# Optimization experiments

Hardware: AMD Instinct MI355X
Metric: run time of the kernel (lower is better)

The kernel has to match this reference:

```python
import jax, jax.numpy as jnp
from jax import lax
import numpy as np

B, S, MEL = 64, 1024, 60
H, L = 180, 4
FS = 3          # mel_smooth_filter_size (num shifted conv branches)
BLOCKS = 3      # mel_smooth_layers
G = MEL // FS   # 20 output units per grouped conv
POST, OUT = 8192, 300


def setup_inputs() -> dict:
    key = jax.random.key(0)
    ks = jax.random.split(key, 13)
    rn = lambda k, shape, s: jax.random.normal(k, shape, jnp.float32) * s
    x = jax.random.normal(ks[0], (B, S, MEL), jnp.float32)
    lens = jax.random.randint(ks[1], (B,), 1, S + 1)
    conv_w = rn(ks[2], (BLOCKS, FS, G, FS, 5), 0.2)   # per block, per shift: (O=20, I/g=3, k=5)
    conv_b = rn(ks[3], (BLOCKS, FS, G), 0.1)
    lstm_wih0 = rn(ks[4], (4 * H, MEL), 0.08)
    lstm_wih_rest = rn(ks[5], (L - 1, 4 * H, H), 0.08)
    lstm_whh = rn(ks[6], (L, 4 * H, H), 0.08)
    lstm_bih = rn(ks[7], (L, 4 * H), 0.05)
    lstm_bhh = rn(ks[8], (L, 4 * H), 0.05)
    post_w = rn(ks[9], (POST, H), 0.05)
    post_b = rn(ks[10], (POST,), 0.05)
    up_w = rn(ks[11], (OUT, POST), 0.02)
    up_b = rn(ks[12], (OUT,), 0.02)
    return dict(x=x, lens=lens, conv_w=conv_w, conv_b=conv_b,
                lstm_wih0=lstm_wih0, lstm_wih_rest=lstm_wih_rest, lstm_whh=lstm_whh,
                lstm_bih=lstm_bih, lstm_bhh=lstm_bhh,
                post_w=post_w, post_b=post_b, up_w=up_w, up_b=up_b)


def _mel_block(xc, w, b):
    # xc: (B, MEL, S); w: (FS, G, FS, 5); b: (FS, G)
    zrow = jnp.zeros_like(xc[:, :1])
    xs = []
    for i in range(FS - 2):  # shift channels down by i+1
        n = i + 1
        xs.append(jnp.concatenate([jnp.zeros_like(xc[:, :n]), xc[:, :-n]], axis=1))
    xs.append(xc)
    xs.append(jnp.concatenate([xc[:, 1:], zrow], axis=1))  # shift channels up by 1
    outs = []
    for j in range(FS):
        o = lax.conv_general_dilated(xs[j], w[j], (1,), [(2, 2)],
                                     dimension_numbers=('NCH', 'OIH', 'NCH'),
                                     feature_group_count=G)
        outs.append(o + b[j][None, :, None])  # (B, G, S)
    # interleave: out channel FS*i + j = outs[j][:, i]
    return jnp.stack(outs, axis=2).reshape(xc.shape[0], MEL, xc.shape[2])


def _lstm_layer(h_in, wih, whh, bih, bhh):
    # h_in: (B, T, I). Torch gate order: i, f, g, o.
    pre = jnp.einsum('bti,gi->btg', h_in, wih) + (bih + bhh)  # (B, T, 4H)
    pre = pre.transpose(1, 0, 2)  # (T, B, 4H)
    h0 = jnp.zeros((h_in.shape[0], H), h_in.dtype)

    def step(carry, p):
        hh, cc = carry
        gates = p + hh @ whh.T
        i, f, g, o = jnp.split(gates, 4, axis=-1)
        cc = jax.nn.sigmoid(f) * cc + jax.nn.sigmoid(i) * jnp.tanh(g)
        hh = jax.nn.sigmoid(o) * jnp.tanh(cc)
        return (hh, cc), hh

    _, outs = lax.scan(step, (h0, h0), pre)
    return outs.transpose(1, 0, 2)  # (B, T, H)


def reference(x, lens, conv_w, conv_b, lstm_wih0, lstm_wih_rest, lstm_whh,
              lstm_bih, lstm_bhh, post_w, post_b, up_w, up_b):
    xc = x.transpose(0, 2, 1)  # (B, MEL, S)
    for blk in range(BLOCKS):
        shortcut = xc
        xc = _mel_block(xc, conv_w[blk], conv_b[blk]) + shortcut  # resid activation = Identity
    h = xc.transpose(0, 2, 1)  # (B, S, MEL)
    for l in range(L):
        wih = lstm_wih0 if l == 0 else lstm_wih_rest[l - 1]
        h = _lstm_layer(h, wih, lstm_whh[l], lstm_bih[l], lstm_bhh[l])
    idx = jnp.clip(lens - 1, 0, S - 1)
    last = h[jnp.arange(h.shape[0]), idx]  # (B, H)
    post = jax.nn.leaky_relu(last @ post_w.T + post_b, 0.01)  # LeakyReLU default slope
    return post @ up_w.T + up_b  # (B, OUT)
```

## Files before the change

### kernel.cpp

```cpp
#include <hip/hip_runtime.h>
#include <hip/hip_fp16.h>

#define BB 64
#define SS 1024
#define MEL 60
#define HH 180
#define G4 720
#define G4P 768
#define NCG 48
#define NKS 6
#define KP 192
#define NL 4
#define NPOST 8192
#define NOUT 300
#define NOUTP 320
#define KSPL 16
#define TT 128
#define CH 64
#define NCH (SS / CH)
#define KPAIR 96

typedef _Float16 f16x8 __attribute__((ext_vector_type(8)));
typedef float f32x4 __attribute__((ext_vector_type(4)));

#if defined(__has_builtin)
#if __has_builtin(__builtin_amdgcn_fdot2)
#define HAVE_FDOT2 1
#endif
#if __has_builtin(__builtin_amdgcn_rcpf)
#define HAVE_RCPF 1
#endif
#endif
#ifndef HAVE_FDOT2
#define HAVE_FDOT2 0
#endif
#ifndef HAVE_RCPF
#define HAVE_RCPF 0
#endif

__device__ __forceinline__ float fdot2u(unsigned int w, unsigned int h, float acc) {
#if HAVE_FDOT2
    typedef _Float16 h2_t __attribute__((ext_vector_type(2)));
    union U { unsigned int u; h2_t v; };
    U a, b;
    a.u = w; b.u = h;
    return __builtin_amdgcn_fdot2(a.v, b.v, acc, false);
#else
    __half2 aw = *reinterpret_cast<const __half2*>(&w);
    __half2 ah = *reinterpret_cast<const __half2*>(&h);
    acc += __half2float(__low2half(aw)) * __half2float(__low2half(ah));
    acc += __half2float(__high2half(aw)) * __half2float(__high2half(ah));
    return acc;
#endif
}

__device__ __forceinline__ float fast_rcp(float x) {
#if HAVE_RCPF
    return __builtin_amdgcn_rcpf(x);
#else
    return 1.f / x;
#endif
}
__device__ __forceinline__ float fsigm(float x) { return fast_rcp(1.f + __expf(-x)); }
__device__ __forceinline__ float ftanh(float x) { return 1.f - 2.f * fast_rcp(__expf(2.f * x) + 1.f); }

union WU { uint4 u; f16x8 f; };

__global__ void prep_wmf(const float* __restrict__ whh, uint4* __restrict__ wmf) {
    int idx = blockIdx.x * blockDim.x + threadIdx.x;
    int total = NL * NCG * NKS * 64;
    if (idx >= total) return;
    int l = idx / (NCG * NKS * 64);
    int r = idx % (NCG * NKS * 64);
    int cg = r / (NKS * 64);
    int r2 = r % (NKS * 64);
    int ks = r2 / 64, lane = r2 % 64;
    int col = cg * 16 + (lane & 15);
    unsigned short v[8];
    #pragma unroll
    for (int j = 0; j < 8; ++j) {
        int k = ks * 32 + ((lane >> 4) << 3) + j;
        float f = (k < HH && col < G4) ? whh[((size_t)l * G4 + col) * HH + k] : 0.f;
        v[j] = __half_as_ushort(__float2half(f));
    }
    uint4 u;
    u.x = (unsigned)v[0] | ((unsigned)v[1] << 16);
    u.y = (unsigned)v[2] | ((unsigned)v[3] << 16);
    u.z = (unsigned)v[4] | ((unsigned)v[5] << 16);
    u.w = (unsigned)v[6] | ((unsigned)v[7] << 16);
    wmf[idx] = u;
}

__global__ void prep_wih16(const float* __restrict__ wih0, const float* __restrict__ wih_rest,
                           unsigned int* __restrict__ w) {
    int idx = blockIdx.x * blockDim.x + threadIdx.x;
    int total = NL * G4 * KPAIR;
    if (idx >= total) return;
    int l = idx / (G4 * KPAIR);
    int r = idx % (G4 * KPAIR);
    int g = r / KPAIR, kp = r % KPAIR;
    int K = (l == 0) ? MEL : HH;
    const float* src = (l == 0) ? (wih0 + (size_t)g * MEL)
                                : (wih_rest + ((size_t)(l - 1) * G4 + g) * HH);
    float a = 0.f, b = 0.f;
    if (2 * kp < K) { a = src[2 * kp]; b = src[2 * kp + 1]; }
    __half2 h2 = __floats2half2_rn(a, b);
    w[idx] = *(unsigned int*)&h2;
}

__global__ void prep_bsum(const float* __restrict__ bih, const float* __restrict__ bhh,
                          float* __restrict__ bsum) {
    int idx = blockIdx.x * blockDim.x + threadIdx.x;
    if (idx >= NL * G4) return;
    bsum[idx] = bih[idx] + bhh[idx];
}

template <typename TIN>
__global__ __launch_bounds__(256) void mel_block(const TIN* __restrict__ in,
                                                 __half* __restrict__ out,
                                                 const float* __restrict__ w,
                                                 const float* __restrict__ bias) {
    __shared__ float xt[TT + 4][MEL];
    __shared__ float ws[900];
    __shared__ float bs[MEL];
    int bb = blockIdx.x;
    int t0 = blockIdx.y * TT;
    int tid = threadIdx.x;
    const TIN* inb = in + (size_t)bb * SS * MEL;
    for (int idx = tid; idx < (TT + 4) * MEL; idx += 256) {
        int tt = idx / MEL, ch = idx % MEL;
        int t = t0 + tt - 2;
        xt[tt][ch] = (t >= 0 && t < SS) ? (float)inb[(size_t)t * MEL + ch] : 0.f;
    }
    for (int idx = tid; idx < 900; idx += 256) ws[idx] = w[idx];
    if (tid < MEL) bs[tid] = bias[(tid % 3) * 20 + tid / 3];
    __syncthreads();
    for (int idx = tid; idx < TT * MEL; idx += 256) {
        int tt = idx / MEL, ch = idx % MEL;
        int i = ch / 3, j = ch % 3;
        int qb = 3 * i + (j - 1);
        float acc = bs[ch];
        #pragma unroll
        for (int c = 0; c < 3; ++c) {
            int q = qb + c;
            if (q >= 0 && q < MEL) {
                const float* wp = ws + ((j * 20 + i) * 3 + c) * 5;
                #pragma unroll
                for (int k = 0; k < 5; ++k) acc += xt[tt + k][q] * wp[k];
            }
        }
        out[(size_t)bb * SS * MEL + (size_t)(t0 + tt) * MEL + ch] =
            __float2half(acc + xt[tt + 2][ch]);
    }
}

struct GemmArgs {
    const __half* A[16];
    const unsigned int* W[16];
    const float* bs[16];
    __half* C[16];
    size_t cbs[16];
    int K[16];
    int KT[16];
    int t0[16];
};

__global__ __launch_bounds__(256) void gemm_pre(GemmArgs ga) {
    int j = blockIdx.z;
    int K = ga.K[j], KT = ga.KT[j];
    const __half* Ab = ga.A[j] + ((size_t)blockIdx.x * SS + ga.t0[j]) * K;
    __half* Cb = ga.C[j] + (size_t)blockIdx.x * ga.cbs[j];
    const unsigned int* Wj = ga.W[j];
    const float* bsum = ga.bs[j];
    __shared__ unsigned int A16[8][72];
    __shared__ unsigned int W16[8][72];
    int n0 = blockIdx.y * 64;
    int tid = threadIdx.x;
    int tx = tid & 15, ty = tid >> 4;
    int kpl = tid & 7, mg = tid >> 3;
    float acc[4][4];
    #pragma unroll
    for (int i = 0; i < 4; ++i)
        #pragma unroll
        for (int jn = 0; jn < 4; ++jn) acc[i][jn] = 0.f;

    for (int kt = 0; kt < KT; ++kt) {
        int kp = kt * 8 + kpl;
        #pragma unroll
        for (int r = 0; r < 2; ++r) {
            int m = mg + 32 * r;
            unsigned int av = 0u;
            if (2 * kp < K) av = *(const unsigned int*)(Ab + (size_t)m * K + 2 * kp);
            A16[kpl][m] = av;
            int g = n0 + m;
            W16[kpl][m] = (g < G4) ? Wj[(size_t)g * KPAIR + kp] : 0u;
        }
        __syncthreads();
        #pragma unroll
        for (int k = 0; k < 8; ++k) {
            unsigned int a[4], b[4];
            #pragma unroll
            for (int i = 0; i < 4; ++i) a[i] = A16[k][ty + (i << 4)];
            #pragma unroll
            for (int jn = 0; jn < 4; ++jn) b[jn] = W16[k][(tx << 2) + jn];
            #pragma unroll
            for (int i = 0; i < 4; ++i)
                #pragma unroll
                for (int jn = 0; jn < 4; ++jn) acc[i][jn] = fdot2u(b[jn], a[i], acc[i][jn]);
        }
        __syncthreads();
    }
    int g0 = n0 + (tx << 2);
    if (g0 < G4) {
        #pragma unroll
        for (int i = 0; i < 4; ++i) {
            int m = ty + (i << 4);
            __half2 p0 = __floats2half2_rn(acc[i][0] + bsum[g0], acc[i][1] + bsum[g0 + 1]);
            __half2 p1 = __floats2half2_rn(acc[i][2] + bsum[g0 + 2], acc[i][3] + bsum[g0 + 3]);
            *(__half2*)(Cb + (size_t)m * G4 + g0) = p0;
            *(__half2*)(Cb + (size_t)m * G4 + g0 + 2) = p1;
        }
    }
}

struct ScanArgs {
    const __half* pre[NL];
    size_t pbs[NL];
    const uint4* wmf[NL];
    __half* hout[NL];
    float* hst[NL];
    float* cst[NL];
    int t0[NL];
};

__global__ __launch_bounds__(768) __attribute__((amdgpu_waves_per_eu(3, 3)))
void lstm_scan(ScanArgs sa) {
    int j = blockIdx.x / BB, b = blockIdx.x % BB;
    int tid = threadIdx.x;
    int wv = tid >> 6, lane = tid & 63;
    int t0 = sa.t0[j];
    const __half* preb = sa.pre[j] + (size_t)b * sa.pbs[j];
    const uint4* wmf = sa.wmf[j];
    __half* houtb = sa.hout[j] + ((size_t)b * SS + (size_t)t0) * HH;
    float* hstb = sa.hst[j] + b * HH;
    float* cstb = sa.cst[j] + b * HH;

    __shared__ __align__(16) unsigned short hs[KP];
    __shared__ float gates[G4P];

    uint4 wfr[24];
    #pragma unroll
    for (int q = 0; q < 4; ++q)
        #pragma unroll
        for (int ks = 0; ks < NKS; ++ks)
            wfr[q * NKS + ks] = wmf[(((size_t)(wv * 4 + q)) * NKS + ks) * 64 + lane];
    #pragma unroll
    for (int r = 0; r < 24; ++r)
        asm volatile("" : "+v"(wfr[r].x), "+v"(wfr[r].y), "+v"(wfr[r].z), "+v"(wfr[r].w));

    float c = 0.f, hlast = 0.f;
    if (tid < KP) {
        float hv = 0.f;
        if (t0 > 0 && tid < HH) { hv = hstb[tid]; c = cstb[tid]; }
        hs[tid] = __half_as_ushort(__float2half(hv));
    }
    __syncthreads();

    float pc0 = 0.f, pc1 = 0.f, pc2 = 0.f, pc3 = 0.f;
    if (tid < HH) {
        pc0 = __half2float(preb[tid]);
        pc1 = __half2float(preb[HH + tid]);
        pc2 = __half2float(preb[2 * HH + tid]);
        pc3 = __half2float(preb[3 * HH + tid]);
    }

    int hoff = (lane >> 4) << 4;
    for (int t = 0; t < CH; ++t) {
        float pn0 = 0.f, pn1 = 0.f, pn2 = 0.f, pn3 = 0.f;
        if (tid < HH && t + 1 < CH) {
            const __half* pp = preb + (size_t)(t + 1) * G4 + tid;
            pn0 = __half2float(pp[0]);
            pn1 = __half2float(pp[HH]);
            pn2 = __half2float(pp[2 * HH]);
            pn3 = __half2float(pp[3 * HH]);
        }
        f16x8 hf[NKS];
        #pragma unroll
        for (int ks = 0; ks < NKS; ++ks) {
            WU hu;
            hu.u = *(const uint4*)((const char*)hs + ks * 64 + hoff);
            hf[ks] = hu.f;
        }
        f32x4 acc0 = {0.f, 0.f, 0.f, 0.f}, acc1 = acc0, acc2 = acc0, acc3 = acc0;
        #pragma unroll
        for (int ks = 0; ks < NKS; ++ks) {
            WU w0, w1, w2, w3;
            w0.u = wfr[0 * NKS + ks]; w1.u = wfr[1 * NKS + ks];
            w2.u = wfr[2 * NKS + ks]; w3.u = wfr[3 * NKS + ks];
            acc0 = __builtin_amdgcn_mfma_f32_16x16x32_f16(hf[ks], w0.f, acc0, 0, 0, 0);
            acc1 = __builtin_amdgcn_mfma_f32_16x16x32_f16(hf[ks], w1.f, acc1, 0, 0, 0);
            acc2 = __builtin_amdgcn_mfma_f32_16x16x32_f16(hf[ks], w2.f, acc2, 0, 0, 0);
            acc3 = __builtin_amdgcn_mfma_f32_16x16x32_f16(hf[ks], w3.f, acc3, 0, 0, 0);
        }
        if (lane < 16) {
            gates[(wv * 4 + 0) * 16 + lane] = acc0[0];
            gates[(wv * 4 + 1) * 16 + lane] = acc1[0];
            gates[(wv * 4 + 2) * 16 + lane] = acc2[0];
            gates[(wv * 4 + 3) * 16 + lane] = acc3[0];
        }
        __syncthreads();
        if (tid < HH) {
            float gi = gates[tid] + pc0;
            float gf = gates[HH + tid] + pc1;
            float gg = gates[2 * HH + tid] + pc2;
            float go = gates[3 * HH + tid] + pc3;
            float si = fsigm(gi);
            float sf = fsigm(gf);
            float so = fsigm(go);
            float tg = ftanh(gg);
            c = sf * c + si * tg;
            float hn = so * ftanh(c);
            __half hh = __float2half(hn);
            hs[tid] = __half_as_ushort(hh);
            hlast = __half2float(hh);
            houtb[(size_t)t * HH + tid] = hh;
        }
        __syncthreads();
        pc0 = pn0; pc1 = pn1; pc2 = pn2; pc3 = pn3;
    }
    if (tid < HH) { hstb[tid] = hlast; cstb[tid] = c; }
}

__global__ void gather_last(const __half* __restrict__ hfin, const int* __restrict__ lens,
                            float* __restrict__ last) {
    int idx = blockIdx.x * blockDim.x + threadIdx.x;
    if (idx >= BB * HH) return;
    int b = idx / HH, d = idx % HH;
    int t = lens[b] - 1;
    t = t < 0 ? 0 : (t > SS - 1 ? SS - 1 : t);
    last[idx] = __half2float(hfin[((size_t)b * SS + t) * HH + d]);
}

__global__ __launch_bounds__(256) void post_gemm(const float* __restrict__ A,
                                                 const float* __restrict__ Bw,
                                                 const float* __restrict__ pb,
                                                 float* __restrict__ Cb) {
    __shared__ float As[16][68];
    __shared__ float Bs[16][68];
    int n0 = blockIdx.x * 64;
    int tid = threadIdx.x;
    int kk = tid & 15, q = tid >> 4;
    int tx = tid & 15, ty = tid >> 4;
    float acc[4][4];
    #pragma unroll
    for (int i = 0; i < 4; ++i)
        #pragma unroll
        for (int jj = 0; jj < 4; ++jj) acc[i][jj] = 0.f;
    for (int kt = 0; kt < 12; ++kt) {
        int kidx = kt * 16 + kk;
        bool kval = kidx < HH;
        #pragma unroll
        for (int r = 0; r < 4; ++r)
            As[kk][q + (r << 4)] = kval ? A[(size_t)(q + (r << 4)) * HH + kidx] : 0.f;
        #pragma unroll
        for (int r = 0; r < 4; ++r)
            Bs[kk][q + (r << 4)] = kval ? Bw[(size_t)(n0 + q + (r << 4)) * HH + kidx] : 0.f;
        __syncthreads();
        #pragma unroll
        for (int k = 0; k < 16; ++k) {
            float a[4], bv[4];
            #pragma unroll
            for (int i = 0; i < 4; ++i) a[i] = As[k][ty + (i << 4)];
            #pragma unroll
            for (int jj = 0; jj < 4; ++jj) bv[jj] = Bs[k][(tx << 2) + jj];
            #pragma unroll
            for (int i = 0; i < 4; ++i)
                #pragma unroll
                for (int jj = 0; jj < 4; ++jj) acc[i][jj] = fmaf(a[i], bv[jj], acc[i][jj]);
        }
        __syncthreads();
    }
    #pragma unroll
    for (int i = 0; i < 4; ++i) {
        int m = ty + (i << 4);
        #pragma unroll
        for (int jj = 0; jj < 4; ++jj) {
            int g = n0 + (tx << 2) + jj;
            float v = acc[i][jj] + pb[g];
            Cb[(size_t)m * NPOST + g] = v > 0.f ? v : 0.01f * v;
        }
    }
}

__global__ __launch_bounds__(256) void up_gemm(const float* __restrict__ A,
                                               const float* __restrict__ Bw,
                                               float* __restrict__ part) {
    __shared__ float As[16][68];
    __shared__ float Bs[16][68];
    int n0 = blockIdx.x * 64;
    int k0 = blockIdx.y * (NPOST / KSPL);
    float* Pb = part + (size_t)blockIdx.y * BB * NOUTP;
    int tid = threadIdx.x;
    int kk = tid & 15, q = tid >> 4;
    int tx = tid & 15, ty = tid >> 4;
    float acc[4][4];
    #pragma unroll
    for (int i = 0; i < 4; ++i)
        #pragma unroll
        for (int jj = 0; jj < 4; ++jj) acc[i][jj] = 0.f;
    for (int kt = 0; kt < (NPOST / KSPL) / 16; ++kt) {
        int kidx = k0 + kt * 16 + kk;
        #pragma unroll
        for (int r = 0; r < 4; ++r)
            As[kk][q + (r << 4)] = A[(size_t)(q + (r << 4)) * NPOST + kidx];
        #pragma unroll
        for (int r = 0; r < 4; ++r) {
            int g = n0 + q + (r << 4);
            Bs[kk][q + (r << 4)] = (g < NOUT) ? Bw[(size_t)g * NPOST + kidx] : 0.f;
        }
        __syncthreads();
        #pragma unroll
        for (int k = 0; k < 16; ++k) {
            float a[4], bv[4];
            #pragma unroll
            for (int i = 0; i < 4; ++i) a[i] = As[k][ty + (i << 4)];
            #pragma unroll
            for (int jj = 0; jj < 4; ++jj) bv[jj] = Bs[k][(tx << 2) + jj];
            #pragma unroll
            for (int i = 0; i < 4; ++i)
                #pragma unroll
                for (int jj = 0; jj < 4; ++jj) acc[i][jj] = fmaf(a[i], bv[jj], acc[i][jj]);
        }
        __syncthreads();
    }
    #pragma unroll
    for (int i = 0; i < 4; ++i) {
        int m = ty + (i << 4);
        #pragma unroll
        for (int jj = 0; jj < 4; ++jj) {
            int g = n0 + (tx << 2) + jj;
            Pb[(size_t)m * NOUTP + g] = acc[i][jj];
        }
    }
}

__global__ void up_reduce(const float* __restrict__ part, const float* __restrict__ ub,
                          float* __restrict__ out) {
    int idx = blockIdx.x * blockDim.x + threadIdx.x;
    if (idx >= BB * NOUT) return;
    int b = idx / NOUT, o = idx % NOUT;
    float acc = ub[o];
    #pragma unroll
    for (int ks = 0; ks < KSPL; ++ks)
        acc += part[((size_t)ks * BB + b) * NOUTP + o];
    out[(size_t)b * NOUT + o] = acc;
}

extern "C" void kernel_launch(void* const* d_in, const int* in_sizes, int n_in,
                              void* d_out, int out_size, void* d_ws, size_t ws_size,
                              hipStream_t stream) {
    const float* x        = (const float*)d_in[0];
    const int*   lens     = (const int*)d_in[1];
    const float* conv_w   = (const float*)d_in[2];
    const float* conv_b   = (const float*)d_in[3];
    const float* wih0     = (const float*)d_in[4];
    const float* wih_rest = (const float*)d_in[5];
    const float* whh      = (const float*)d_in[6];
    const float* bih      = (const float*)d_in[7];
    const float* bhh      = (const float*)d_in[8];
    const float* post_w   = (const float*)d_in[9];
    const float* post_b   = (const float*)d_in[10];
    const float* up_w     = (const float*)d_in[11];
    const float* up_b     = (const float*)d_in[12];
    float* out = (float*)d_out;
    (void)in_sizes; (void)n_in; (void)out_size;

    auto pad = [](size_t v) { return (v + 255) & ~(size_t)255; };
    const size_t szMel   = (size_t)BB * SS * MEL * 2;
    const size_t szH     = (size_t)BB * SS * HH * 2;
    const size_t szPre0  = (size_t)BB * SS * G4 * 2;
    const size_t szSlot  = (size_t)BB * CH * G4 * 2;
    const size_t szWmf   = (size_t)NL * NCG * NKS * 64 * 16;
    const size_t szWih   = (size_t)NL * G4 * KPAIR * 4;
    const size_t szBsum  = (size_t)NL * G4 * 4;
    const size_t szState = (size_t)NL * BB * HH * 4;
    const size_t szLast  = (size_t)BB * HH * 4;
    const size_t szPost  = (size_t)BB * NPOST * 4;
    const size_t szPart  = (size_t)KSPL * BB * NOUTP * 4;

    size_t commonSmall = pad(szWmf) + pad(szWih) + pad(szBsum) + 2 * pad(szState) +
                         pad(szLast) + pad(szPost) + pad(szPart) + 4096;
    size_t need1 = pad(szMel) + 4 * pad(szH) + pad(szPre0) + 3 * pad(szSlot) + commonSmall;
    size_t need2 = pad(szMel) + 4 * pad(szH) + 4 * pad(szSlot) + commonSmall;
    int tier = (ws_size >= need1) ? 1 : ((ws_size >= need2) ? 2 : 3);

    char* wsp = (char*)d_ws;
    size_t off = 0;
    auto alloc = [&](size_t bytes) -> void* {
        void* p = wsp + off;
        off = (off + bytes + 255) & ~(size_t)255;
        return p;
    };

    __half* melF = (__half*)alloc(szMel);
    __half* hbuf[NL];
    if (tier <= 2) {
        for (int l = 0; l < NL; ++l) hbuf[l] = (__half*)alloc(szH);
    } else {
        __half* p0 = (__half*)alloc(szH);
        __half* p1 = (__half*)alloc(szH);
        hbuf[0] = p0; hbuf[1] = p1; hbuf[2] = p0; hbuf[3] = p1;
    }
    __half* pre0 = nullptr;
    __half* slot[NL] = {nullptr, nullptr, nullptr, nullptr};
    if (tier == 1) {
        pre0 = (__half*)alloc(szPre0);
        for (int l = 1; l < NL; ++l) slot[l] = (__half*)alloc(szSlot);
    } else if (tier == 2) {
        for (int l = 0; l < NL; ++l) slot[l] = (__half*)alloc(szSlot);
    } else {
        slot[0] = (__half*)alloc(szSlot);
        for (int l = 1; l < NL; ++l) slot[l] = slot[0];
    }
    uint4* wmf = (uint4*)alloc(szWmf);
    unsigned int* wih16 = (unsigned int*)alloc(szWih);
    float* bsum  = (float*)alloc(szBsum);
    float* hstates = (float*)alloc(szState);
    float* cstates = (float*)alloc(szState);
    float* lastb = (float*)alloc(szLast);
    float* postb = (float*)alloc(szPost);
    float* partb = (float*)alloc(szPart);

    prep_wmf<<<(NL * NCG * NKS * 64 + 255) / 256, 256, 0, stream>>>(whh, wmf);
    prep_wih16<<<(NL * G4 * KPAIR + 255) / 256, 256, 0, stream>>>(wih0, wih_rest, wih16);
    prep_bsum<<<(NL * G4 + 255) / 256, 256, 0, stream>>>(bih, bhh, bsum);

    {
        __half* m0 = hbuf[0];
        __half* m1 = (__half*)((char*)hbuf[0] + pad(szMel));
        mel_block<float><<<dim3(BB, SS / TT), 256, 0, stream>>>(x, m0, conv_w + 0 * 900, conv_b + 0 * 60);
        mel_block<__half><<<dim3(BB, SS / TT), 256, 0, stream>>>(m0, m1, conv_w + 1 * 900, conv_b + 1 * 60);
        mel_block<__half><<<dim3(BB, SS / TT), 256, 0, stream>>>(m1, melF, conv_w + 2 * 900, conv_b + 2 * 60);
    }

    auto setGemmJob = [&](GemmArgs& ga, int nj, int l, int c) {
        ga.A[nj]  = (l == 0) ? melF : hbuf[l - 1];
        ga.K[nj]  = (l == 0) ? MEL : HH;
        ga.KT[nj] = (l == 0) ? 4 : 12;
        ga.W[nj]  = wih16 + (size_t)l * G4 * KPAIR;
        ga.bs[nj] = bsum + l * G4;
        if (tier == 1 && l == 0) {
            ga.C[nj] = pre0 + (size_t)c * CH * G4;
            ga.cbs[nj] = (size_t)SS * G4;
        } else {
            ga.C[nj] = slot[l];
            ga.cbs[nj] = (size_t)CH * G4;
        }
        ga.t0[nj] = c * CH;
    };
    auto setScanJob = [&](ScanArgs& sa, int nj, int l, int c) {
        if (tier == 1 && l == 0) {
            sa.pre[nj] = pre0 + (size_t)c * CH * G4;
            sa.pbs[nj] = (size_t)SS * G4;
        } else {
            sa.pre[nj] = slot[l];
            sa.pbs[nj] = (size_t)CH * G4;
        }
        sa.wmf[nj]  = wmf + (size_t)l * NCG * NKS * 64;
        sa.hout[nj] = hbuf[l];
        sa.hst[nj]  = hstates + (size_t)l * BB * HH;
        sa.cst[nj]  = cstates + (size_t)l * BB * HH;
        sa.t0[nj]   = c * CH;
    };

    if (tier <= 2) {
        if (tier == 1) {
            GemmArgs ga{};
            for (int c = 0; c < NCH; ++c) setGemmJob(ga, c, 0, c);
            gemm_pre<<<dim3(BB, 12, NCH), 256, 0, stream>>>(ga);
        }
        int lmin = (tier == 1) ? 1 : 0;
        for (int w = 0; w < NCH + NL - 1; ++w) {
            GemmArgs ga{};
            int njg = 0;
            for (int l = lmin; l < NL; ++l) {
                int c = w - l;
                if (c < 0 || c >= NCH) continue;
                setGemmJob(ga, njg++, l, c);
            }
            if (njg) gemm_pre<<<dim3(BB, 12, njg), 256, 0, stream>>>(ga);
            ScanArgs sa{};
            int njs = 0;
            for (int l = 0; l < NL; ++l) {
                int c = w - l;
                if (c < 0 || c >= NCH) continue;
                setScanJob(sa, njs++, l, c);
            }
            if (njs) lstm_scan<<<dim3(njs * BB), 768, 0, stream>>>(sa);
        }
    } else {
        for (int l = 0; l < NL; ++l) {
            for (int c = 0; c < NCH; ++c) {
                GemmArgs ga{}; ScanArgs sa{};
                setGemmJob(ga, 0, l, c);
                gemm_pre<<<dim3(BB, 12, 1), 256, 0, stream>>>(ga);
                setScanJob(sa, 0, l, c);
                lstm_scan<<<dim3(BB), 768, 0, stream>>>(sa);
            }
        }
    }

    gather_last<<<(BB * HH + 255) / 256, 256, 0, stream>>>(hbuf[NL - 1], lens, lastb);
    post_gemm<<<NPOST / 64, 256, 0, stream>>>(lastb, post_w, post_b, postb);
    up_gemm<<<dim3(NOUTP / 64, KSPL), 256, 0, stream>>>(postb, up_w, partb);
    up_reduce<<<(BB * NOUT + 255) / 256, 256, 0, stream>>>(partb, up_b, out);
}
```

Measured before the change: 2.061 ms.

## Fuse LSTM input projection into scan kernel using MFMA per chunk

Removes the separate fdot2-based gemm_pre kernel and its global pre-activation buffers. Each lstm_scan block now computes its chunk's input projection with MFMA into shared memory, in two halves of 32 timesteps, before running the recurrence. This cuts kernel launches per wavefront step and the global round trip for the pre-activations. In exchange the scan blocks do more work serially, and the shared-memory footprint grows, which may limit occupancy. The layer-0 projection can no longer be precomputed for all chunks up front.

```diff
diff --git a/kernel.cpp b/kernel.cpp
--- a/kernel.cpp
+++ b/kernel.cpp
@@ -18,41 +18,19 @@
 #define TT 128
 #define CH 64
 #define NCH (SS / CH)
-#define KPAIR 96
+#define HCH 32
 
 typedef _Float16 f16x8 __attribute__((ext_vector_type(8)));
 typedef float f32x4 __attribute__((ext_vector_type(4)));
 
 #if defined(__has_builtin)
-#if __has_builtin(__builtin_amdgcn_fdot2)
-#define HAVE_FDOT2 1
-#endif
 #if __has_builtin(__builtin_amdgcn_rcpf)
 #define HAVE_RCPF 1
 #endif
 #endif
-#ifndef HAVE_FDOT2
-#define HAVE_FDOT2 0
-#endif
 #ifndef HAVE_RCPF
 #define HAVE_RCPF 0
 #endif
-
-__device__ __forceinline__ float fdot2u(unsigned int w, unsigned int h, float acc) {
-#if HAVE_FDOT2
-    typedef _Float16 h2_t __attribute__((ext_vector_type(2)));
-    union U { unsigned int u; h2_t v; };
-    U a, b;
-    a.u = w; b.u = h;
-    return __builtin_amdgcn_fdot2(a.v, b.v, acc, false);
-#else
-    __half2 aw = *reinterpret_cast<const __half2*>(&w);
-    __half2 ah = *reinterpret_cast<const __half2*>(&h);
-    acc += __half2float(__low2half(aw)) * __half2float(__low2half(ah));
-    acc += __half2float(__high2half(aw)) * __half2float(__high2half(ah));
-    return acc;
-#endif
-}
 
 __device__ __forceinline__ float fast_rcp(float x) {
 #if HAVE_RCPF
@@ -62,7 +40,7 @@
 #endif
 }
 __device__ __forceinline__ float fsigm(float x) { return fast_rcp(1.f + __expf(-x)); }
-__device__ __forceinline__ float ftanh(float x) { return 1.f - 2.f * fast_rcp(__expf(2.f * x) + 1.f); }
+__device__ __forceinline__ float ftanh_(float x) { return 1.f - 2.f * fast_rcp(__expf(2.f * x) + 1.f); }
 
 union WU { uint4 u; f16x8 f; };
 
@@ -91,21 +69,34 @@
     wmf[idx] = u;
 }
 
-__global__ void prep_wih16(const float* __restrict__ wih0, const float* __restrict__ wih_rest,
-                           unsigned int* __restrict__ w) {
+__global__ void prep_wmfI(const float* __restrict__ wih0, const float* __restrict__ wih_rest,
+                          uint4* __restrict__ wmfI) {
     int idx = blockIdx.x * blockDim.x + threadIdx.x;
-    int total = NL * G4 * KPAIR;
+    int total = NL * NCG * NKS * 64;
     if (idx >= total) return;
-    int l = idx / (G4 * KPAIR);
-    int r = idx % (G4 * KPAIR);
-    int g = r / KPAIR, kp = r % KPAIR;
+    int l = idx / (NCG * NKS * 64);
+    int r = idx % (NCG * NKS * 64);
+    int cg = r / (NKS * 64);
+    int r2 = r % (NKS * 64);
+    int ks = r2 / 64, lane = r2 % 64;
+    int col = cg * 16 + (lane & 15);
     int K = (l == 0) ? MEL : HH;
-    const float* src = (l == 0) ? (wih0 + (size_t)g * MEL)
-                                : (wih_rest + ((size_t)(l - 1) * G4 + g) * HH);
-    float a = 0.f, b = 0.f;
-    if (2 * kp < K) { a = src[2 * kp]; b = src[2 * kp + 1]; }
-    __half2 h2 = __floats2half2_rn(a, b);
-    w[idx] = *(unsigned int*)&h2;
+    unsigned short v[8];
+    #pragma unroll
+    for (int j = 0; j < 8; ++j) {
+        int k = ks * 32 + ((lane >> 4) << 3) + j;
+        float f = 0.f;
+        if (col < G4 && k < K)
+            f = (l == 0) ? wih0[(size_t)col * MEL + k]
+                         : wih_rest[((size_t)(l - 1) * G4 + col) * HH + k];
+        v[j] = __half_as_ushort(__float2half(f));
+    }
+    uint4 u;
+    u.x = (unsigned)v[0] | ((unsigned)v[1] << 16);
+    u.y = (unsigned)v[2] | ((unsigned)v[3] << 16);
+    u.z = (unsigned)v[4] | ((unsigned)v[5] << 16);
+    u.w = (unsigned)v[6] | ((unsigned)v[7] << 16);
+    wmfI[idx] = u;
 }
 
 __global__ void prep_bsum(const float* __restrict__ bih, const float* __restrict__ bhh,
@@ -154,97 +145,36 @@
     }
 }
 
-struct GemmArgs {
-    const __half* A[16];
-    const unsigned int* W[16];
-    const float* bs[16];
-    __half* C[16];
-    size_t cbs[16];
-    int K[16];
-    int KT[16];
-    int t0[16];
-};
-
-__global__ __launch_bounds__(256) void gemm_pre(GemmArgs ga) {
-    int j = blockIdx.z;
-    int K = ga.K[j], KT = ga.KT[j];
-    const __half* Ab = ga.A[j] + ((size_t)blockIdx.x * SS + ga.t0[j]) * K;
-    __half* Cb = ga.C[j] + (size_t)blockIdx.x * ga.cbs[j];
-    const unsigned int* Wj = ga.W[j];
-    const float* bsum = ga.bs[j];
-    __shared__ unsigned int A16[8][72];
-    __shared__ unsigned int W16[8][72];
-    int n0 = blockIdx.y * 64;
-    int tid = threadIdx.x;
-    int tx = tid & 15, ty = tid >> 4;
-    int kpl = tid & 7, mg = tid >> 3;
-    float acc[4][4];
-    #pragma unroll
-    for (int i = 0; i < 4; ++i)
-        #pragma unroll
-        for (int jn = 0; jn < 4; ++jn) acc[i][jn] = 0.f;
-
-    for (int kt = 0; kt < KT; ++kt) {
-        int kp = kt * 8 + kpl;
-        #pragma unroll
-        for (int r = 0; r < 2; ++r) {
-            int m = mg + 32 * r;
-            unsigned int av = 0u;
-            if (2 * kp < K) av = *(const unsigned int*)(Ab + (size_t)m * K + 2 * kp);
-            A16[kpl][m] = av;
-            int g = n0 + m;
-            W16[kpl][m] = (g < G4) ? Wj[(size_t)g * KPAIR + kp] : 0u;
-        }
-        __syncthreads();
-        #pragma unroll
-        for (int k = 0; k < 8; ++k) {
-            unsigned int a[4], b[4];
-            #pragma unroll
-            for (int i = 0; i < 4; ++i) a[i] = A16[k][ty + (i << 4)];
-            #pragma unroll
-            for (int jn = 0; jn < 4; ++jn) b[jn] = W16[k][(tx << 2) + jn];
-            #pragma unroll
-            for (int i = 0; i < 4; ++i)
-                #pragma unroll
-                for (int jn = 0; jn < 4; ++jn) acc[i][jn] = fdot2u(b[jn], a[i], acc[i][jn]);
-        }
-        __syncthreads();
-    }
-    int g0 = n0 + (tx << 2);
-    if (g0 < G4) {
-        #pragma unroll
-        for (int i = 0; i < 4; ++i) {
-            int m = ty + (i << 4);
-            __half2 p0 = __floats2half2_rn(acc[i][0] + bsum[g0], acc[i][1] + bsum[g0 + 1]);
-            __half2 p1 = __floats2half2_rn(acc[i][2] + bsum[g0 + 2], acc[i][3] + bsum[g0 + 3]);
-            *(__half2*)(Cb + (size_t)m * G4 + g0) = p0;
-            *(__half2*)(Cb + (size_t)m * G4 + g0 + 2) = p1;
-        }
-    }
-}
-
 struct ScanArgs {
-    const __half* pre[NL];
-    size_t pbs[NL];
-    const uint4* wmf[NL];
-    __half* hout[NL];
-    float* hst[NL];
-    float* cst[NL];
-    int t0[NL];
+    const __half* A[NL];
+    const uint4*  wmfi[NL];
+    const uint4*  wmf[NL];
+    const float*  bs[NL];
+    __half*       hout[NL];
+    float*        hst[NL];
+    float*        cst[NL];
+    int           K[NL];
+    int           t0[NL];
 };
 
 __global__ __launch_bounds__(768) __attribute__((amdgpu_waves_per_eu(3, 3)))
 void lstm_scan(ScanArgs sa) {
-    int j = blockIdx.x / BB, b = blockIdx.x % BB;
+    int j = blockIdx.x >> 6, b = blockIdx.x & 63;
     int tid = threadIdx.x;
     int wv = tid >> 6, lane = tid & 63;
+    int r0 = lane >> 4, cl = lane & 15;
     int t0 = sa.t0[j];
-    const __half* preb = sa.pre[j] + (size_t)b * sa.pbs[j];
+    int K = sa.K[j];
+    const __half* Ab = sa.A[j] + ((size_t)b * SS + t0) * K;
+    const uint4* wmfI = sa.wmfi[j];
     const uint4* wmf = sa.wmf[j];
+    const float* bsum = sa.bs[j];
     __half* houtb = sa.hout[j] + ((size_t)b * SS + (size_t)t0) * HH;
     float* hstb = sa.hst[j] + b * HH;
     float* cstb = sa.cst[j] + b * HH;
 
+    __shared__ __align__(16) unsigned short A_lds[HCH][200];
+    __shared__ __align__(16) unsigned short preL[HCH][728];
     __shared__ __align__(16) unsigned short hs[KP];
     __shared__ float gates[G4P];
 
@@ -264,69 +194,86 @@
         if (t0 > 0 && tid < HH) { hv = hstb[tid]; c = cstb[tid]; }
         hs[tid] = __half_as_ushort(__float2half(hv));
     }
-    __syncthreads();
-
-    float pc0 = 0.f, pc1 = 0.f, pc2 = 0.f, pc3 = 0.f;
-    if (tid < HH) {
-        pc0 = __half2float(preb[tid]);
-        pc1 = __half2float(preb[HH + tid]);
-        pc2 = __half2float(preb[2 * HH + tid]);
-        pc3 = __half2float(preb[3 * HH + tid]);
-    }
-
-    int hoff = (lane >> 4) << 4;
-    for (int t = 0; t < CH; ++t) {
-        float pn0 = 0.f, pn1 = 0.f, pn2 = 0.f, pn3 = 0.f;
-        if (tid < HH && t + 1 < CH) {
-            const __half* pp = preb + (size_t)(t + 1) * G4 + tid;
-            pn0 = __half2float(pp[0]);
-            pn1 = __half2float(pp[HH]);
-            pn2 = __half2float(pp[2 * HH]);
-            pn3 = __half2float(pp[3 * HH]);
-        }
-        f16x8 hf[NKS];
-        #pragma unroll
-        for (int ks = 0; ks < NKS; ++ks) {
-            WU hu;
-            hu.u = *(const uint4*)((const char*)hs + ks * 64 + hoff);
-            hf[ks] = hu.f;
-        }
-        f32x4 acc0 = {0.f, 0.f, 0.f, 0.f}, acc1 = acc0, acc2 = acc0, acc3 = acc0;
-        #pragma unroll
-        for (int ks = 0; ks < NKS; ++ks) {
-            WU w0, w1, w2, w3;
-            w0.u = wfr[0 * NKS + ks]; w1.u = wfr[1 * NKS + ks];
-            w2.u = wfr[2 * NKS + ks]; w3.u = wfr[3 * NKS + ks];
-            acc0 = __builtin_amdgcn_mfma_f32_16x16x32_f16(hf[ks], w0.f, acc0, 0, 0, 0);
-            acc1 = __builtin_amdgcn_mfma_f32_16x16x32_f16(hf[ks], w1.f, acc1, 0, 0, 0);
-            acc2 = __builtin_amdgcn_mfma_f32_16x16x32_f16(hf[ks], w2.f, acc2, 0, 0, 0);
-            acc3 = __builtin_amdgcn_mfma_f32_16x16x32_f16(hf[ks], w3.f, acc3, 0, 0, 0);
-        }
-        if (lane < 16) {
-            gates[(wv * 4 + 0) * 16 + lane] = acc0[0];
-            gates[(wv * 4 + 1) * 16 + lane] = acc1[0];
-            gates[(wv * 4 + 2) * 16 + lane] = acc2[0];
-            gates[(wv * 4 + 3) * 16 + lane] = acc3[0];
-        }
-        __syncthreads();
-        if (tid < HH) {
-            float gi = gates[tid] + pc0;
-            float gf = gates[HH + tid] + pc1;
-            float gg = gates[2 * HH + tid] + pc2;
-            float go = gates[3 * HH + tid] + pc3;
-            float si = fsigm(gi);
-            float sf = fsigm(gf);
-            float so = fsigm(go);
-            float tg = ftanh(gg);
-            c = sf * c + si * tg;
-            float hn = so * ftanh(c);
-            __half hh = __float2half(hn);
-            hs[tid] = __half_as_ushort(hh);
-            hlast = __half2float(hh);
-            houtb[(size_t)t * HH + tid] = hh;
-        }
-        __syncthreads();
-        pc0 = pn0; pc1 = pn1; pc2 = pn2; pc3 = pn3;
+
+    int hoff = r0 << 4;
+    for (int half = 0; half < 2; ++half) {
+        __syncthreads();
+        for (int idx = tid; idx < HCH * 100; idx += 768) {
+            int row = idx / 100, kp2 = idx % 100;
+            unsigned v = 0u;
+            if (2 * kp2 < K)
+                v = *(const unsigned*)(Ab + (size_t)(half * HCH + row) * K + 2 * kp2);
+            *(unsigned*)&A_lds[row][2 * kp2] = v;
+        }
+        __syncthreads();
+        #pragma unroll
+        for (int mt = 0; mt < 2; ++mt) {
+            #pragma unroll
+            for (int q = 0; q < 4; ++q) {
+                int cgg = wv * 4 + q;
+                int col = cgg * 16 + cl;
+                f32x4 acc = {0.f, 0.f, 0.f, 0.f};
+                for (int ks = 0; ks < NKS; ++ks) {
+                    WU af, wB;
+                    af.u = *(const uint4*)((const char*)&A_lds[(mt << 4) + cl][0] + (ks << 6) + (r0 << 4));
+                    wB.u = wmfI[((size_t)cgg * NKS + ks) * 64 + lane];
+                    acc = __builtin_amdgcn_mfma_f32_16x16x32_f16(af.f, wB.f, acc, 0, 0, 0);
+                }
+                if (col < G4) {
+                    float bv = bsum[col];
+                    #pragma unroll
+                    for (int i = 0; i < 4; ++i) {
+                        int tl = (mt << 4) + (r0 << 2) + i;
+                        preL[tl][col] = __half_as_ushort(__float2half(acc[i] + bv));
+                    }
+                }
+            }
+        }
+        __syncthreads();
+        for (int tt = 0; tt < HCH; ++tt) {
+            f16x8 hf[NKS];
+            #pragma unroll
+            for (int ks = 0; ks < NKS; ++ks) {
+                WU hu;
+                hu.u = *(const uint4*)((const char*)hs + (ks << 6) + hoff);
+                hf[ks] = hu.f;
+            }
+            f32x4 a0 = {0.f,0.f,0.f,0.f}, a1 = a0, a2 = a0, a3 = a0;
+            #pragma unroll
+            for (int ks = 0; ks < NKS; ++ks) {
+                WU w0, w1, w2, w3;
+                w0.u = wfr[0 * NKS + ks]; w1.u = wfr[1 * NKS + ks];
+                w2.u = wfr[2 * NKS + ks]; w3.u = wfr[3 * NKS + ks];
+                a0 = __builtin_amdgcn_mfma_f32_16x16x32_f16(hf[ks], w0.f, a0, 0, 0, 0);
+                a1 = __builtin_amdgcn_mfma_f32_16x16x32_f16(hf[ks], w1.f, a1, 0, 0, 0);
+                a2 = __builtin_amdgcn_mfma_f32_16x16x32_f16(hf[ks], w2.f, a2, 0, 0, 0);
+                a3 = __builtin_amdgcn_mfma_f32_16x16x32_f16(hf[ks], w3.f, a3, 0, 0, 0);
+            }
+            if (lane < 16) {
+                gates[(wv * 4 + 0) * 16 + lane] = a0[0];
+                gates[(wv * 4 + 1) * 16 + lane] = a1[0];
+                gates[(wv * 4 + 2) * 16 + lane] = a2[0];
+                gates[(wv * 4 + 3) * 16 + lane] = a3[0];
+            }
+            __syncthreads();
+            if (tid < HH) {
+                float gi = gates[tid]          + __half2float(__ushort_as_half(preL[tt][tid]));
+                float gf = gates[HH + tid]     + __half2float(__ushort_as_half(preL[tt][HH + tid]));
+                float gg = gates[2 * HH + tid] + __half2float(__ushort_as_half(preL[tt][2 * HH + tid]));
+                float go = gates[3 * HH + tid] + __half2float(__ushort_as_half(preL[tt][3 * HH + tid]));
+                float si = fsigm(gi);
+                float sf = fsigm(gf);
+                float so = fsigm(go);
+                float tg = ftanh_(gg);
+                c = sf * c + si * tg;
+                float hn = so * ftanh_(c);
+                __half hh = __float2half(hn);
+                hs[tid] = __half_as_ushort(hh);
+                hlast = __half2float(hh);
+                houtb[(size_t)(half * HCH + tt) * HH + tid] = hh;
+            }
+            __syncthreads();
+        }
     }
     if (tid < HH) { hstb[tid] = hlast; cstb[tid] = c; }
 }
@@ -478,21 +425,17 @@
     auto pad = [](size_t v) { return (v + 255) & ~(size_t)255; };
     const size_t szMel   = (size_t)BB * SS * MEL * 2;
     const size_t szH     = (size_t)BB * SS * HH * 2;
-    const size_t szPre0  = (size_t)BB * SS * G4 * 2;
-    const size_t szSlot  = (size_t)BB * CH * G4 * 2;
     const size_t szWmf   = (size_t)NL * NCG * NKS * 64 * 16;
-    const size_t szWih   = (size_t)NL * G4 * KPAIR * 4;
     const size_t szBsum  = (size_t)NL * G4 * 4;
     const size_t szState = (size_t)NL * BB * HH * 4;
     const size_t szLast  = (size_t)BB * HH * 4;
     const size_t szPost  = (size_t)BB * NPOST * 4;
     const size_t szPart  = (size_t)KSPL * BB * NOUTP * 4;
 
-    size_t commonSmall = pad(szWmf) + pad(szWih) + pad(szBsum) + 2 * pad(szState) +
+    size_t commonSmall = 2 * pad(szWmf) + pad(szBsum) + 2 * pad(szState) +
                          pad(szLast) + pad(szPost) + pad(szPart) + 4096;
-    size_t need1 = pad(szMel) + 4 * pad(szH) + pad(szPre0) + 3 * pad(szSlot) + commonSmall;
-    size_t need2 = pad(szMel) + 4 * pad(szH) + 4 * pad(szSlot) + commonSmall;
-    int tier = (ws_size >= need1) ? 1 : ((ws_size >= need2) ? 2 : 3);
+    size_t needWF = pad(szMel) + 4 * pad(szH) + commonSmall;
+    int wavefront = (ws_size >= needWF) ? 1 : 0;
 
     char* wsp = (char*)d_ws;
     size_t off = 0;
@@ -504,26 +447,15 @@
 
     __half* melF = (__half*)alloc(szMel);
     __half* hbuf[NL];
-    if (tier <= 2) {
+    if (wavefront) {
         for (int l = 0; l < NL; ++l) hbuf[l] = (__half*)alloc(szH);
     } else {
         __half* p0 = (__half*)alloc(szH);
         __half* p1 = (__half*)alloc(szH);
         hbuf[0] = p0; hbuf[1] = p1; hbuf[2] = p0; hbuf[3] = p1;
     }
-    __half* pre0 = nullptr;
-    __half* slot[NL] = {nullptr, nullptr, nullptr, nullptr};
-    if (tier == 1) {
-        pre0 = (__half*)alloc(szPre0);
-        for (int l = 1; l < NL; ++l) slot[l] = (__half*)alloc(szSlot);
-    } else if (tier == 2) {
-        for (int l = 0; l < NL; ++l) slot[l] = (__half*)alloc(szSlot);
-    } else {
-        slot[0] = (__half*)alloc(szSlot);
-        for (int l = 1; l < NL; ++l) slot[l] = slot[0];
-    }
-    uint4* wmf = (uint4*)alloc(szWmf);
-    unsigned int* wih16 = (unsigned int*)alloc(szWih);
+    uint4* wmf  = (uint4*)alloc(szWmf);
+    uint4* wmfI = (uint4*)alloc(szWmf);
     float* bsum  = (float*)alloc(szBsum);
     float* hstates = (float*)alloc(szState);
     float* cstates = (float*)alloc(szState);
@@ -532,7 +464,7 @@
     float* partb = (float*)alloc(szPart);
 
     prep_wmf<<<(NL * NCG * NKS * 64 + 255) / 256, 256, 0, stream>>>(whh, wmf);
-    prep_wih16<<<(NL * G4 * KPAIR + 255) / 256, 256, 0, stream>>>(wih0, wih_rest, wih16);
+    prep_wmfI<<<(NL * NCG * NKS * 64 + 255) / 256, 256, 0, stream>>>(wih0, wih_rest, wmfI);
     prep_bsum<<<(NL * G4 + 255) / 256, 256, 0, stream>>>(bih, bhh, bsum);
 
     {
@@ -543,68 +475,34 @@
         mel_block<__half><<<dim3(BB, SS / TT), 256, 0, stream>>>(m1, melF, conv_w + 2 * 900, conv_b + 2 * 60);
     }
 
-    auto setGemmJob = [&](GemmArgs& ga, int nj, int l, int c) {
-        ga.A[nj]  = (l == 0) ? melF : hbuf[l - 1];
-        ga.K[nj]  = (l == 0) ? MEL : HH;
-        ga.KT[nj] = (l == 0) ? 4 : 12;
-        ga.W[nj]  = wih16 + (size_t)l * G4 * KPAIR;
-        ga.bs[nj] = bsum + l * G4;
-        if (tier == 1 && l == 0) {
-            ga.C[nj] = pre0 + (size_t)c * CH * G4;
-            ga.cbs[nj] = (size_t)SS * G4;
-        } else {
-            ga.C[nj] = slot[l];
-            ga.cbs[nj] = (size_t)CH * G4;
-        }
-        ga.t0[nj] = c * CH;
-    };
-    auto setScanJob = [&](ScanArgs& sa, int nj, int l, int c) {
-        if (tier == 1 && l == 0) {
-            sa.pre[nj] = pre0 + (size_t)c * CH * G4;
-            sa.pbs[nj] = (size_t)SS * G4;
-        } else {
-            sa.pre[nj] = slot[l];
-            sa.pbs[nj] = (size_t)CH * G4;
-        }
+    auto setJob = [&](ScanArgs& sa, int nj, int l, int c) {
+        sa.A[nj]    = (l == 0) ? melF : hbuf[l - 1];
+        sa.K[nj]    = (l == 0) ? MEL : HH;
+        sa.wmfi[nj] = wmfI + (size_t)l * NCG * NKS * 64;
         sa.wmf[nj]  = wmf + (size_t)l * NCG * NKS * 64;
+        sa.bs[nj]   = bsum + l * G4;
         sa.hout[nj] = hbuf[l];
         sa.hst[nj]  = hstates + (size_t)l * BB * HH;
         sa.cst[nj]  = cstates + (size_t)l * BB * HH;
         sa.t0[nj]   = c * CH;
     };
 
-    if (tier <= 2) {
-        if (tier == 1) {
-            GemmArgs ga{};
-            for (int c = 0; c < NCH; ++c) setGemmJob(ga, c, 0, c);
-            gemm_pre<<<dim3(BB, 12, NCH), 256, 0, stream>>>(ga);
-        }
-        int lmin = (tier == 1) ? 1 : 0;
+    if (wavefront) {
         for (int w = 0; w < NCH + NL - 1; ++w) {
-            GemmArgs ga{};
-            int njg = 0;
-            for (int l = lmin; l < NL; ++l) {
-                int c = w - l;
-                if (c < 0 || c >= NCH) continue;
-                setGemmJob(ga, njg++, l, c);
-            }
-            if (njg) gemm_pre<<<dim3(BB, 12, njg), 256, 0, stream>>>(ga);
             ScanArgs sa{};
             int njs = 0;
             for (int l = 0; l < NL; ++l) {
                 int c = w - l;
                 if (c < 0 || c >= NCH) continue;
-                setScanJob(sa, njs++, l, c);
+                setJob(sa, njs++, l, c);
             }
             if (njs) lstm_scan<<<dim3(njs * BB), 768, 0, stream>>>(sa);
         }
     } else {
         for (int l = 0; l < NL; ++l) {
             for (int c = 0; c < NCH; ++c) {
-                GemmArgs ga{}; ScanArgs sa{};
-                setGemmJob(ga, 0, l, c);
-                gemm_pre<<<dim3(BB, 12, 1), 256, 0, stream>>>(ga);
-                setScanJob(sa, 0, l, c);
+                ScanArgs sa{};
+                setJob(sa, 0, l, c);
                 lstm_scan<<<dim3(BB), 768, 0, stream>>>(sa);
             }
         }
```

Measured after the change: 2.113 ms. +2.5%, slower.

## Use MFMA f16 matrix cores for LSTM input-projection GEMM with LDS-staged output

Applied to the files above, without the earlier changes.

Replaces the scalar fdot2-based input-projection GEMM with MFMA 16x16x32 f16 instructions. The input weights are pre-packed into the same per-lane fragment layout already used for the recurrent weights. Each block stages its whole 64-row activation tile in LDS once, and writes results through an LDS buffer so global stores are 16-byte vectors. This removes the per-k-tile syncs and FMA-bound inner loop, at the cost of a larger LDS footprint and an extra packed-weight buffer.

```diff
diff --git a/kernel.cpp b/kernel.cpp
--- a/kernel.cpp
+++ b/kernel.cpp
@@ -18,41 +18,18 @@
 #define TT 128
 #define CH 64
 #define NCH (SS / CH)
-#define KPAIR 96
 
 typedef _Float16 f16x8 __attribute__((ext_vector_type(8)));
 typedef float f32x4 __attribute__((ext_vector_type(4)));
 
 #if defined(__has_builtin)
-#if __has_builtin(__builtin_amdgcn_fdot2)
-#define HAVE_FDOT2 1
-#endif
 #if __has_builtin(__builtin_amdgcn_rcpf)
 #define HAVE_RCPF 1
 #endif
 #endif
-#ifndef HAVE_FDOT2
-#define HAVE_FDOT2 0
-#endif
 #ifndef HAVE_RCPF
 #define HAVE_RCPF 0
 #endif
-
-__device__ __forceinline__ float fdot2u(unsigned int w, unsigned int h, float acc) {
-#if HAVE_FDOT2
-    typedef _Float16 h2_t __attribute__((ext_vector_type(2)));
-    union U { unsigned int u; h2_t v; };
-    U a, b;
-    a.u = w; b.u = h;
-    return __builtin_amdgcn_fdot2(a.v, b.v, acc, false);
-#else
-    __half2 aw = *reinterpret_cast<const __half2*>(&w);
-    __half2 ah = *reinterpret_cast<const __half2*>(&h);
-    acc += __half2float(__low2half(aw)) * __half2float(__low2half(ah));
-    acc += __half2float(__high2half(aw)) * __half2float(__high2half(ah));
-    return acc;
-#endif
-}
 
 __device__ __forceinline__ float fast_rcp(float x) {
 #if HAVE_RCPF
@@ -91,21 +68,34 @@
     wmf[idx] = u;
 }
 
-__global__ void prep_wih16(const float* __restrict__ wih0, const float* __restrict__ wih_rest,
-                           unsigned int* __restrict__ w) {
+__global__ void prep_wmfI(const float* __restrict__ wih0, const float* __restrict__ wih_rest,
+                          uint4* __restrict__ wmfI) {
     int idx = blockIdx.x * blockDim.x + threadIdx.x;
-    int total = NL * G4 * KPAIR;
+    int total = NL * NCG * NKS * 64;
     if (idx >= total) return;
-    int l = idx / (G4 * KPAIR);
-    int r = idx % (G4 * KPAIR);
-    int g = r / KPAIR, kp = r % KPAIR;
+    int l = idx / (NCG * NKS * 64);
+    int r = idx % (NCG * NKS * 64);
+    int cg = r / (NKS * 64);
+    int r2 = r % (NKS * 64);
+    int ks = r2 / 64, lane = r2 % 64;
+    int col = cg * 16 + (lane & 15);
     int K = (l == 0) ? MEL : HH;
-    const float* src = (l == 0) ? (wih0 + (size_t)g * MEL)
-                                : (wih_rest + ((size_t)(l - 1) * G4 + g) * HH);
-    float a = 0.f, b = 0.f;
-    if (2 * kp < K) { a = src[2 * kp]; b = src[2 * kp + 1]; }
-    __half2 h2 = __floats2half2_rn(a, b);
-    w[idx] = *(unsigned int*)&h2;
+    unsigned short v[8];
+    #pragma unroll
+    for (int j = 0; j < 8; ++j) {
+        int k = ks * 32 + ((lane >> 4) << 3) + j;
+        float f = 0.f;
+        if (col < G4 && k < K)
+            f = (l == 0) ? wih0[(size_t)col * MEL + k]
+                         : wih_rest[((size_t)(l - 1) * G4 + col) * HH + k];
+        v[j] = __half_as_ushort(__float2half(f));
+    }
+    uint4 u;
+    u.x = (unsigned)v[0] | ((unsigned)v[1] << 16);
+    u.y = (unsigned)v[2] | ((unsigned)v[3] << 16);
+    u.z = (unsigned)v[4] | ((unsigned)v[5] << 16);
+    u.w = (unsigned)v[6] | ((unsigned)v[7] << 16);
+    wmfI[idx] = u;
 }
 
 __global__ void prep_bsum(const float* __restrict__ bih, const float* __restrict__ bhh,
@@ -156,69 +146,72 @@
 
 struct GemmArgs {
     const __half* A[16];
-    const unsigned int* W[16];
-    const float* bs[16];
-    __half* C[16];
-    size_t cbs[16];
-    int K[16];
-    int KT[16];
-    int t0[16];
+    const uint4*  W[16];
+    const float*  bs[16];
+    __half*       C[16];
+    size_t        cbs[16];
+    int           K[16];
+    int           kts[16];
+    int           t0[16];
 };
 
 __global__ __launch_bounds__(256) void gemm_pre(GemmArgs ga) {
     int j = blockIdx.z;
-    int K = ga.K[j], KT = ga.KT[j];
+    int K = ga.K[j], KTS = ga.kts[j];
     const __half* Ab = ga.A[j] + ((size_t)blockIdx.x * SS + ga.t0[j]) * K;
     __half* Cb = ga.C[j] + (size_t)blockIdx.x * ga.cbs[j];
-    const unsigned int* Wj = ga.W[j];
+    const uint4* WB = ga.W[j];
     const float* bsum = ga.bs[j];
-    __shared__ unsigned int A16[8][72];
-    __shared__ unsigned int W16[8][72];
     int n0 = blockIdx.y * 64;
+    int cg0 = blockIdx.y * 4;
+    __shared__ __align__(16) unsigned short A_lds[64][200];
+    __shared__ __align__(16) unsigned short outb[64][68];
     int tid = threadIdx.x;
-    int tx = tid & 15, ty = tid >> 4;
-    int kpl = tid & 7, mg = tid >> 3;
-    float acc[4][4];
-    #pragma unroll
-    for (int i = 0; i < 4; ++i)
-        #pragma unroll
-        for (int jn = 0; jn < 4; ++jn) acc[i][jn] = 0.f;
-
-    for (int kt = 0; kt < KT; ++kt) {
-        int kp = kt * 8 + kpl;
-        #pragma unroll
-        for (int r = 0; r < 2; ++r) {
-            int m = mg + 32 * r;
-            unsigned int av = 0u;
-            if (2 * kp < K) av = *(const unsigned int*)(Ab + (size_t)m * K + 2 * kp);
-            A16[kpl][m] = av;
-            int g = n0 + m;
-            W16[kpl][m] = (g < G4) ? Wj[(size_t)g * KPAIR + kp] : 0u;
-        }
-        __syncthreads();
-        #pragma unroll
-        for (int k = 0; k < 8; ++k) {
-            unsigned int a[4], b[4];
-            #pragma unroll
-            for (int i = 0; i < 4; ++i) a[i] = A16[k][ty + (i << 4)];
-            #pragma unroll
-            for (int jn = 0; jn < 4; ++jn) b[jn] = W16[k][(tx << 2) + jn];
-            #pragma unroll
-            for (int i = 0; i < 4; ++i)
-                #pragma unroll
-                for (int jn = 0; jn < 4; ++jn) acc[i][jn] = fdot2u(b[jn], a[i], acc[i][jn]);
-        }
-        __syncthreads();
-    }
-    int g0 = n0 + (tx << 2);
-    if (g0 < G4) {
+    int wv = tid >> 6, lane = tid & 63;
+    int r0 = lane >> 4, cl = lane & 15;
+
+    int npair = KTS << 4;
+    for (int idx = tid; idx < (npair << 6); idx += 256) {
+        int row = idx / npair, p = idx % npair;
+        unsigned v = 0u;
+        if (2 * p < K) v = *(const unsigned*)(Ab + (size_t)row * K + 2 * p);
+        *(unsigned*)&A_lds[row][2 * p] = v;
+    }
+    __syncthreads();
+
+    const unsigned short* arow = &A_lds[(wv << 4) + cl][0];
+    #pragma unroll
+    for (int q = 0; q < 4; ++q) {
+        int cg = cg0 + q;
+        f32x4 acc = {0.f, 0.f, 0.f, 0.f};
+        for (int ks = 0; ks < KTS; ++ks) {
+            WU af, wB;
+            af.u = *(const uint4*)((const char*)arow + (ks << 6) + (r0 << 4));
+            wB.u = WB[((size_t)cg * NKS + ks) * 64 + lane];
+            acc = __builtin_amdgcn_mfma_f32_16x16x32_f16(af.f, wB.f, acc, 0, 0, 0);
+        }
+        int col = cg * 16 + cl;
+        float bv = (col < G4) ? bsum[col] : 0.f;
+        int cloc = (q << 4) + cl;
         #pragma unroll
         for (int i = 0; i < 4; ++i) {
-            int m = ty + (i << 4);
-            __half2 p0 = __floats2half2_rn(acc[i][0] + bsum[g0], acc[i][1] + bsum[g0 + 1]);
-            __half2 p1 = __floats2half2_rn(acc[i][2] + bsum[g0 + 2], acc[i][3] + bsum[g0 + 3]);
-            *(__half2*)(Cb + (size_t)m * G4 + g0) = p0;
-            *(__half2*)(Cb + (size_t)m * G4 + g0 + 2) = p1;
+            int row = (wv << 4) + (r0 << 2) + i;
+            outb[row][cloc] = __half_as_ushort(__float2half(acc[i] + bv));
+        }
+    }
+    __syncthreads();
+    for (int idx = tid; idx < 64 * 8; idx += 256) {
+        int row = idx >> 3, seg = idx & 7;
+        int colg = n0 + (seg << 3);
+        if (colg + 7 < G4) {
+            uint4 val = *(const uint4*)&outb[row][seg << 3];
+            *(uint4*)(Cb + (size_t)row * G4 + colg) = val;
+        } else {
+            for (int e = 0; e < 8; ++e) {
+                int cg2 = colg + e;
+                if (cg2 < G4)
+                    Cb[(size_t)row * G4 + cg2] = __ushort_as_half(outb[row][(seg << 3) + e]);
+            }
         }
     }
 }
@@ -481,14 +474,13 @@
     const size_t szPre0  = (size_t)BB * SS * G4 * 2;
     const size_t szSlot  = (size_t)BB * CH * G4 * 2;
     const size_t szWmf   = (size_t)NL * NCG * NKS * 64 * 16;
-    const size_t szWih   = (size_t)NL * G4 * KPAIR * 4;
     const size_t szBsum  = (size_t)NL * G4 * 4;
     const size_t szState = (size_t)NL * BB * HH * 4;
     const size_t szLast  = (size_t)BB * HH * 4;
     const size_t szPost  = (size_t)BB * NPOST * 4;
     const size_t szPart  = (size_t)KSPL * BB * NOUTP * 4;
 
-    size_t commonSmall = pad(szWmf) + pad(szWih) + pad(szBsum) + 2 * pad(szState) +
+    size_t commonSmall = 2 * pad(szWmf) + pad(szBsum) + 2 * pad(szState) +
                          pad(szLast) + pad(szPost) + pad(szPart) + 4096;
     size_t need1 = pad(szMel) + 4 * pad(szH) + pad(szPre0) + 3 * pad(szSlot) + commonSmall;
     size_t need2 = pad(szMel) + 4 * pad(szH) + 4 * pad(szSlot) + commonSmall;
@@ -522,8 +514,8 @@
         slot[0] = (__half*)alloc(szSlot);
         for (int l = 1; l < NL; ++l) slot[l] = slot[0];
     }
-    uint4* wmf = (uint4*)alloc(szWmf);
-    unsigned int* wih16 = (unsigned int*)alloc(szWih);
+    uint4* wmf  = (uint4*)alloc(szWmf);
+    uint4* wmfI = (uint4*)alloc(szWmf);
     float* bsum  = (float*)alloc(szBsum);
     float* hstates = (float*)alloc(szState);
     float* cstates = (float*)alloc(szState);
@@ -532,7 +524,7 @@
     float* partb = (float*)alloc(szPart);
 
     prep_wmf<<<(NL * NCG * NKS * 64 + 255) / 256, 256, 0, stream>>>(whh, wmf);
-    prep_wih16<<<(NL * G4 * KPAIR + 255) / 256, 256, 0, stream>>>(wih0, wih_rest, wih16);
+    prep_wmfI<<<(NL * NCG * NKS * 64 + 255) / 256, 256, 0, stream>>>(wih0, wih_rest, wmfI);
     prep_bsum<<<(NL * G4 + 255) / 256, 256, 0, stream>>>(bih, bhh, bsum);
 
     {
@@ -544,11 +536,11 @@
     }
 
     auto setGemmJob = [&](GemmArgs& ga, int nj, int l, int c) {
-        ga.A[nj]  = (l == 0) ? melF : hbuf[l - 1];
-        ga.K[nj]  = (l == 0) ? MEL : HH;
-        ga.KT[nj] = (l == 0) ? 4 : 12;
-        ga.W[nj]  = wih16 + (size_t)l * G4 * KPAIR;
-        ga.bs[nj] = bsum + l * G4;
+        ga.A[nj]   = (l == 0) ? melF : hbuf[l - 1];
+        ga.K[nj]   = (l == 0) ? MEL : HH;
+        ga.kts[nj] = (l == 0) ? 2 : 6;
+        ga.W[nj]   = wmfI + (size_t)l * NCG * NKS * 64;
+        ga.bs[nj]  = bsum + l * G4;
         if (tier == 1 && l == 0) {
             ga.C[nj] = pre0 + (size_t)c * CH * G4;
             ga.cbs[nj] = (size_t)SS * G4;
```

New measurement: 2.093 ms. No clear change (+1.5%).
